# Kernel optimization log

Hardware: AMD Instinct MI355X
Metric: run time of the kernel (lower is better)

The kernel has to match this reference:

```python
import jax, jax.numpy as jnp
import numpy as np

N = 100000      # nodes
E = 1000000     # edges (before self loops)
F_IN = 128      # num_features
G = 512         # graphs in batch
NC = 10         # num_classes
EPS_BN = 1e-5
NEG_SLOPE = 0.2


def setup_inputs() -> dict:
    key = jax.random.key(0)
    ks = iter(jax.random.split(key, 40))
    rn = lambda shape, s=0.1: jax.random.normal(next(ks), shape, jnp.float32) * s
    inp = {
        "x": jax.random.normal(next(ks), (N, F_IN), jnp.float32),
        "edge_index": jax.random.randint(next(ks), (2, E), 0, N),
        "batch": jnp.sort(jax.random.randint(next(ks), (N,), 0, G)),
        "W1": rn((F_IN, 128)), "as1": rn((8, 16)), "ad1": rn((8, 16)), "b1": jnp.zeros((128,), jnp.float32),
        "g1": jnp.ones((128,), jnp.float32), "be1": jnp.zeros((128,), jnp.float32),
        "Wl1": rn((128, 16)), "bl1": jnp.zeros((16,), jnp.float32),
        "gl1": jnp.ones((16,), jnp.float32), "bel1": jnp.zeros((16,), jnp.float32),
        "W2": rn((16, 96)), "as2": rn((4, 24)), "ad2": rn((4, 24)), "b2": jnp.zeros((96,), jnp.float32),
        "g2": jnp.ones((96,), jnp.float32), "be2": jnp.zeros((96,), jnp.float32),
        "Wl2": rn((96, 24)), "bl2": jnp.zeros((24,), jnp.float32),
        "gl2": jnp.ones((24,), jnp.float32), "bel2": jnp.zeros((24,), jnp.float32),
        "W3": rn((24, 64)), "as3": rn((2, 32)), "ad3": rn((2, 32)), "b3": jnp.zeros((64,), jnp.float32),
        "g3": jnp.ones((64,), jnp.float32), "be3": jnp.zeros((64,), jnp.float32),
        # final classifier
        "Wo": rn((64, NC)), "bo": jnp.zeros((NC,), jnp.float32),
    }
    return inp


def _bn(h, gamma, beta):
    # training-mode BatchNorm1d: batch statistics, biased variance
    m = jnp.mean(h, axis=0)
    v = jnp.var(h, axis=0)
    return gamma * (h - m) * jax.lax.rsqrt(v + EPS_BN) + beta


def _gat(h_in, src, dst, W, a_src, a_dst, bias, n):
    heads, ch = a_src.shape
    h = (h_in @ W).reshape(n, heads, ch)                     # [N,H,C]
    alpha_s = jnp.sum(h * a_src, axis=-1)                    # [N,H]
    alpha_d = jnp.sum(h * a_dst, axis=-1)                    # [N,H]
    e = jax.nn.leaky_relu(alpha_s[src] + alpha_d[dst], NEG_SLOPE)   # [E,H]
    emax = jax.ops.segment_max(e, dst, num_segments=n)       # segment softmax over target
    e = jnp.exp(e - emax[dst])
    denom = jax.ops.segment_sum(e, dst, num_segments=n)
    alpha = e / (denom[dst] + 1e-16)                         # [E,H]
    msg = h[src] * alpha[:, :, None]                         # [E,H,C]
    out = jax.ops.segment_sum(msg, dst, num_segments=n)      # [N,H,C]
    return out.reshape(n, heads * ch) + bias


def reference(x, edge_index, batch,
              W1, as1, ad1, b1, g1, be1, Wl1, bl1, gl1, bel1,
              W2, as2, ad2, b2, g2, be2, Wl2, bl2, gl2, bel2,
              W3, as3, ad3, b3, g3, be3, Wo, bo):
    n = x.shape[0]
    loop = jnp.arange(n)
    src = jnp.concatenate([edge_index[0], loop])   # add self loops (PyG default)
    dst = jnp.concatenate([edge_index[1], loop])

    h = jax.nn.relu(_bn(_gat(x, src, dst, W1, as1, ad1, b1, n), g1, be1))
    h = jax.nn.relu(_bn(h @ Wl1 + bl1, gl1, bel1))
    h = jax.nn.relu(_bn(_gat(h, src, dst, W2, as2, ad2, b2, n), g2, be2))
    h = jax.nn.relu(_bn(h @ Wl2 + bl2, gl2, bel2))
    h = jax.nn.relu(_bn(_gat(h, src, dst, W3, as3, ad3, b3, n), g3, be3))

    # global mean pool over graphs
    counts = jax.ops.segment_sum(jnp.ones((n,), h.dtype), batch, num_segments=G)
    pooled = jax.ops.segment_sum(h, batch, num_segments=G) / jnp.maximum(counts, 1.0)[:, None]
    # dropout is identity in eval
    return pooled @ Wo + bo
```

## Files before the change

kernel.cpp:

```cpp
#include <hip/hip_runtime.h>

typedef unsigned short u16;
typedef unsigned int   u32;
typedef unsigned long long u64;
typedef __attribute__((ext_vector_type(8))) short short8;
typedef __attribute__((ext_vector_type(4))) float f32x4;

#define DEVI __device__ __forceinline__

#define NPB 256
#define SHB 8
#define BHB 64

DEVI float bf2f(u16 u){ union{u32 i; float f;} x; x.i = ((u32)u)<<16; return x.f; }
DEVI u16 f2bf(float f){ union{float f; u32 i;} x; x.f = f;
  u32 r = (x.i + 0x7FFFu + ((x.i>>16)&1u))>>16; return (u16)r; }
DEVI float lrelu(float x){ return x > 0.f ? x : 0.2f*x; }
DEVI float gload(const void* p, size_t i, int f32){
  return f32 ? ((const float*)p)[i] : bf2f(((const u16*)p)[i]);
}

__global__ __launch_bounds__(256) void k_init(const void* x, int* flag, float* stats, int nst){
  int i = blockIdx.x*256 + threadIdx.x;
  if (i < nst) stats[i] = 0.f;
  if (i == 0){
    const u16* p = (const u16*)x;
    int hits = 0;
    for (int j = 0; j < 512; j++){
      u16 e = (p[j] >> 7) & 0xFF;
      if (e >= 0xC0) hits++;
    }
    *flag = hits ? 1 : 0;
  }
}

__global__ __launch_bounds__(1024) void k_bhist(const int* ei, int E, int* hist, int NB){
  __shared__ int lh[512];
  for (int b = threadIdx.x; b < NB; b += 1024) lh[b] = 0;
  __syncthreads();
  for (int e = blockIdx.x*1024 + threadIdx.x; e < E; e += BHB*1024)
    atomicAdd(&lh[((u32)ei[E + e]) >> SHB], 1);
  __syncthreads();
  for (int b = threadIdx.x; b < NB; b += 1024) hist[blockIdx.x*NB + b] = lh[b];
}

__global__ __launch_bounds__(256) void k_btot(const int* hist, int* tot, int NB){
  int b = blockIdx.x*256 + threadIdx.x;
  if (b < NB){
    int s = 0;
    for (int j = 0; j < BHB; j++) s += hist[j*NB + b];
    tot[b] = s;
  }
}

__global__ __launch_bounds__(1024) void k_bbase(const int* tot, int* base, int* coff, int NB, int N){
  __shared__ int l[1024];
  int t = threadIdx.x;
  int v = (t < NB) ? tot[t] : 0;
  l[t] = v; __syncthreads();
  for (int s = 1; s < 1024; s <<= 1){
    int add = (t >= s) ? l[t - s] : 0;
    __syncthreads();
    l[t] += add;
    __syncthreads();
  }
  if (t < NB) base[t] = l[t] - v;
  if (t == 1023){ base[NB] = l[1023]; coff[N] = l[1023]; }
}

__global__ __launch_bounds__(256) void k_bcur(int* hist, const int* base, int NB){
  int b = blockIdx.x*256 + threadIdx.x;
  if (b < NB){
    int run = base[b];
    for (int j = 0; j < BHB; j++){
      int v = hist[j*NB + b];
      hist[j*NB + b] = run;
      run += v;
    }
  }
}

__global__ __launch_bounds__(1024) void k_bfill(const int* ei, int E, const int* hist,
                                                u64* tmp, int NB){
  __shared__ int cur[512];
  for (int b = threadIdx.x; b < NB; b += 1024) cur[b] = hist[blockIdx.x*NB + b];
  __syncthreads();
  for (int e = blockIdx.x*1024 + threadIdx.x; e < E; e += BHB*1024){
    int s = ei[e], d = ei[E + e];
    int p = atomicAdd(&cur[((u32)d) >> SHB], 1);
    tmp[p] = ((u64)(u32)d << 32) | (u32)s;
  }
}

__global__ __launch_bounds__(256) void k_cfill(const u64* tmp, const int* base,
                                               int* coff, int* csr, int N){
  __shared__ int cnt[NPB], start[NPB];
  int b = blockIdx.x, t = threadIdx.x;
  int p0 = base[b], p1 = base[b + 1];
  cnt[t] = 0;
  __syncthreads();
  for (int i = p0 + t; i < p1; i += 256)
    atomicAdd(&cnt[(int)(tmp[i] >> 32) & (NPB - 1)], 1);
  __syncthreads();
  if (t == 0){
    int run = p0;
    for (int j = 0; j < NPB; j++){ start[j] = run; run += cnt[j]; }
  }
  __syncthreads();
  {
    int node = b*NPB + t;
    if (node < N) coff[node] = start[t];
    cnt[t] = 0;
  }
  __syncthreads();
  for (int i = p0 + t; i < p1; i += 256){
    u64 pr = tmp[i];
    int dj = (int)(pr >> 32) & (NPB - 1);
    int r = atomicAdd(&cnt[dj], 1);
    csr[start[dj] + r] = (int)(u32)pr;
  }
}

__global__ __launch_bounds__(256) void k_prepW(const void* Wg, u16* Wt, const int* dflag){
  const int f32 = dflag[0];
  for (int i = blockIdx.x*256 + threadIdx.x; i < 128*128; i += gridDim.x*256){
    int k = i >> 7, nn = i & 127;
    Wt[nn*128 + k] = f2bf(gload(Wg, i, f32));
  }
}

__global__ __launch_bounds__(256) void k_mfma1(const void* x, const u16* __restrict__ Wt,
                                               u16* __restrict__ out, int n, const int* dflag){
  const int f32 = dflag[0];
  const int wave = threadIdx.x >> 6;
  const int lane = threadIdx.x & 63;
  const int l15 = lane & 15, q = lane >> 4;
  const int arow = blockIdx.x*64 + wave*16 + l15;
  const bool rok = arow < n;

  f32x4 acc[8];
  #pragma unroll
  for (int t = 0; t < 8; t++) acc[t] = {0.f, 0.f, 0.f, 0.f};

  #pragma unroll
  for (int kk = 0; kk < 4; kk++){
    short8 a = {0,0,0,0,0,0,0,0};
    if (rok){
      const int ko = kk*32 + q*8;
      if (f32){
        const float* xp = (const float*)x + (size_t)arow*128 + ko;
        float4 v0 = *(const float4*)xp;
        float4 v1 = *(const float4*)(xp + 4);
        a[0]=(short)f2bf(v0.x); a[1]=(short)f2bf(v0.y); a[2]=(short)f2bf(v0.z); a[3]=(short)f2bf(v0.w);
        a[4]=(short)f2bf(v1.x); a[5]=(short)f2bf(v1.y); a[6]=(short)f2bf(v1.z); a[7]=(short)f2bf(v1.w);
      } else {
        a = *(const short8*)((const u16*)x + (size_t)arow*128 + ko);
      }
    }
    #pragma unroll
    for (int t = 0; t < 8; t++){
      short8 b = *(const short8*)(Wt + (size_t)(l15 + 16*t)*128 + kk*32 + q*8);
      acc[t] = __builtin_amdgcn_mfma_f32_16x16x32_bf16(a, b, acc[t], 0, 0, 0);
    }
  }

  const int orow0 = blockIdx.x*64 + wave*16 + q*4;
  #pragma unroll
  for (int r = 0; r < 4; r++){
    int orow = orow0 + r;
    if (orow < n){
      #pragma unroll
      for (int t = 0; t < 8; t++)
        out[(size_t)orow*128 + l15 + 16*t] = f2bf(acc[t][r]);
    }
  }
}

__global__ __launch_bounds__(256) void k_alpha1(const u16* __restrict__ A, const void* a_s, const void* a_d,
    u16* als, u16* ald, int n, const int* dflag){
  const int f32 = dflag[0];
  int idx = blockIdx.x*256 + threadIdx.x;
  if (idx >= n*8) return;
  int r = idx >> 3, hd = idx & 7;
  const u16* p = A + (size_t)r*128 + hd*16;
  float s = 0.f, d = 0.f;
  #pragma unroll
  for (int c = 0; c < 16; c++){
    float v = bf2f(p[c]);
    s = fmaf(v, gload(a_s, hd*16 + c, f32), s);
    d = fmaf(v, gload(a_d, hd*16 + c, f32), d);
  }
  als[idx] = f2bf(s); ald[idx] = f2bf(d);
}

template<int K,int M,int H,int RT,int TPB,bool AFFINE,bool ALPHA>
__global__ __launch_bounds__(TPB) void k_gemm(
    const u16* in, const void* Wg,
    const float* stat, const void* gam, const void* bet, float invn,
    const void* a_s, const void* a_d, u16* out, u16* als, u16* ald, int n,
    const int* dflag)
{
  constexpr int CT = 4;
  constexpr int TC = M/CT;
  constexpr int TR = TPB/TC;
  constexpr int ROWS = TR*RT;
  constexpr int C = M/H;
  static_assert(TPB % TC == 0, "");
  __shared__ __align__(16) u16 Wl[K*M];
  __shared__ float Il[ROWS*(K+1)];
  __shared__ float red[ALPHA ? (2*ROWS*TC) : 1];
  __shared__ float faL[AFFINE ? K : 1], fdL[AFFINE ? K : 1];

  const int f32 = dflag[0];
  if constexpr (AFFINE){
    for (int k = threadIdx.x; k < K; k += TPB){
      float m = stat[k]*invn;
      float vv = stat[128 + k]*invn - m*m;
      float a = gload(gam, k, f32) * rsqrtf(vv + 1e-5f);
      faL[k] = a;
      fdL[k] = gload(bet, k, f32) - m*a;
    }
    __syncthreads();
  }

  for (int i = threadIdx.x; i < K*M; i += TPB)
    Wl[i] = f32 ? f2bf(((const float*)Wg)[i]) : ((const u16*)Wg)[i];

  const int rowbase = blockIdx.x * ROWS;
  for (int i = threadIdx.x; i < ROWS*K; i += TPB){
    int rr = i / K, k = i - rr*K;
    int r = rowbase + rr;
    float v = 0.f;
    if (r < n){
      v = bf2f(in[(size_t)r*K + k]);
      if constexpr (AFFINE) v = fmaxf(fmaf(faL[k], v, fdL[k]), 0.f);
    }
    Il[rr*(K+1) + k] = v;
  }
  __syncthreads();

  const int tc = threadIdx.x % TC;
  const int tr = threadIdx.x / TC;
  float acc[RT][CT];
  #pragma unroll
  for (int j = 0; j < RT; j++)
    #pragma unroll
    for (int c = 0; c < CT; c++) acc[j][c] = 0.f;

  #pragma unroll 8
  for (int k = 0; k < K; k++){
    ushort4 u = *(const ushort4*)&Wl[k*M + tc*CT];
    float w0 = bf2f(u.x), w1 = bf2f(u.y), w2 = bf2f(u.z), w3 = bf2f(u.w);
    #pragma unroll
    for (int j = 0; j < RT; j++){
      float iv = Il[(tr + j*TR)*(K+1) + k];
      acc[j][0] = fmaf(iv, w0, acc[j][0]);
      acc[j][1] = fmaf(iv, w1, acc[j][1]);
      acc[j][2] = fmaf(iv, w2, acc[j][2]);
      acc[j][3] = fmaf(iv, w3, acc[j][3]);
    }
  }

  #pragma unroll
  for (int j = 0; j < RT; j++){
    int r = rowbase + tr + j*TR;
    if (r < n){
      ushort4 st;
      st.x = f2bf(acc[j][0]); st.y = f2bf(acc[j][1]);
      st.z = f2bf(acc[j][2]); st.w = f2bf(acc[j][3]);
      *(ushort4*)&out[(size_t)r*M + tc*CT] = st;
    }
  }

  if constexpr (ALPHA){
    #pragma unroll
    for (int j = 0; j < RT; j++){
      float ps = 0.f, pd = 0.f;
      #pragma unroll
      for (int c = 0; c < CT; c++){
        ps = fmaf(acc[j][c], gload(a_s, tc*CT + c, f32), ps);
        pd = fmaf(acc[j][c], gload(a_d, tc*CT + c, f32), pd);
      }
      red[(tr + j*TR)*TC + tc] = ps;
      red[ROWS*TC + (tr + j*TR)*TC + tc] = pd;
    }
    __syncthreads();
    if (threadIdx.x < ROWS){
      int r = rowbase + threadIdx.x;
      if (r < n){
        float hs[H], hd[H];
        #pragma unroll
        for (int h = 0; h < H; h++){ hs[h] = 0.f; hd[h] = 0.f; }
        for (int t2 = 0; t2 < TC; t2++){
          int hh = (t2*CT)/C;
          hs[hh] += red[threadIdx.x*TC + t2];
          hd[hh] += red[ROWS*TC + threadIdx.x*TC + t2];
        }
        #pragma unroll
        for (int h = 0; h < H; h++){
          als[(size_t)r*H + h] = f2bf(hs[h]);
          ald[(size_t)r*H + h] = f2bf(hd[h]);
        }
      }
    }
  }
}

template<int H,int C>
__global__ __launch_bounds__(256) void k_pullA(const u16* __restrict__ h,
    const u16* __restrict__ als, const u16* __restrict__ ald,
    const int* __restrict__ off, const int* __restrict__ csr, u16* __restrict__ out, int n)
{
  constexpr int F = H*C;
  constexpr int L = F/2;
  int wid = blockIdx.x*4 + (threadIdx.x >> 6);
  if (wid >= n) return;
  int lane = threadIdx.x & 63;
  if (lane >= L) return;
  int hd = (2*lane)/C;
  float adi = bf2f(ald[(size_t)wid*H + hd]);
  float asi = bf2f(als[(size_t)wid*H + hd]);
  const u32* hw = (const u32*)h;

  float w = __expf(lrelu(asi + adi));
  u32 v = hw[(size_t)wid*L + lane];
  float a0 = w * bf2f((u16)v);
  float a1 = w * bf2f((u16)(v >> 16));
  float den = w;

  int e = off[wid], e1 = off[wid + 1];
  for (; e + 8 <= e1; e += 8){
    int s[8]; float bl[8]; u32 vv[8];
    #pragma unroll
    for (int u = 0; u < 8; u++) s[u] = csr[e + u];
    #pragma unroll
    for (int u = 0; u < 8; u++) bl[u] = bf2f(als[(size_t)s[u]*H + hd]);
    #pragma unroll
    for (int u = 0; u < 8; u++) vv[u] = hw[(size_t)s[u]*L + lane];
    #pragma unroll
    for (int u = 0; u < 8; u++){
      float wu = __expf(lrelu(bl[u] + adi));
      a0 = fmaf(wu, bf2f((u16)vv[u]), a0);
      a1 = fmaf(wu, bf2f((u16)(vv[u] >> 16)), a1);
      den += wu;
    }
  }
  if (e < e1){
    int s[8]; float bl[8]; u32 vv[8];
    #pragma unroll
    for (int u = 0; u < 8; u++){ int idx = e + u; s[u] = csr[idx < e1 ? idx : e]; }
    #pragma unroll
    for (int u = 0; u < 8; u++) bl[u] = bf2f(als[(size_t)s[u]*H + hd]);
    #pragma unroll
    for (int u = 0; u < 8; u++) vv[u] = hw[(size_t)s[u]*L + lane];
    #pragma unroll
    for (int u = 0; u < 8; u++){
      float wu = (e + u < e1) ? __expf(lrelu(bl[u] + adi)) : 0.f;
      a0 = fmaf(wu, bf2f((u16)vv[u]), a0);
      a1 = fmaf(wu, bf2f((u16)(vv[u] >> 16)), a1);
      den += wu;
    }
  }
  float r = 1.f/(den + 1e-16f);
  ((u32*)out)[(size_t)wid*L + lane] = (u32)f2bf(a0*r) | ((u32)f2bf(a1*r) << 16);
}

__global__ __launch_bounds__(256) void k_pullB(const u16* __restrict__ h,
    const u16* __restrict__ als, const u16* __restrict__ ald,
    const int* __restrict__ off, const int* __restrict__ csr, u16* __restrict__ out, int n)
{
  int wid = blockIdx.x*4 + (threadIdx.x >> 6);
  if (wid >= n) return;
  int lane = threadIdx.x & 63;
  int half = lane >> 5, fi = lane & 31;
  int hd = fi >> 4;
  float adi = bf2f(ald[(size_t)wid*2 + hd]);
  float asi = bf2f(als[(size_t)wid*2 + hd]);
  const u32* hw = (const u32*)h;

  float a0 = 0.f, a1 = 0.f, den = 0.f;
  if (half == 0){
    float w = __expf(lrelu(asi + adi));
    u32 v = hw[(size_t)wid*32 + fi];
    a0 = w * bf2f((u16)v);
    a1 = w * bf2f((u16)(v >> 16));
    den = w;
  }
  int e = off[wid] + half, e1 = off[wid + 1];
  for (; e + 6 < e1; e += 8){
    int s[4]; float bl[4]; u32 vv[4];
    #pragma unroll
    for (int u = 0; u < 4; u++) s[u] = csr[e + 2*u];
    #pragma unroll
    for (int u = 0; u < 4; u++) bl[u] = bf2f(als[(size_t)s[u]*2 + hd]);
    #pragma unroll
    for (int u = 0; u < 4; u++) vv[u] = hw[(size_t)s[u]*32 + fi];
    #pragma unroll
    for (int u = 0; u < 4; u++){
      float wu = __expf(lrelu(bl[u] + adi));
      a0 = fmaf(wu, bf2f((u16)vv[u]), a0);
      a1 = fmaf(wu, bf2f((u16)(vv[u] >> 16)), a1);
      den += wu;
    }
  }
  if (e < e1){
    int s[4]; float bl[4]; u32 vv[4];
    #pragma unroll
    for (int u = 0; u < 4; u++){ int idx = e + 2*u; s[u] = csr[idx < e1 ? idx : e]; }
    #pragma unroll
    for (int u = 0; u < 4; u++) bl[u] = bf2f(als[(size_t)s[u]*2 + hd]);
    #pragma unroll
    for (int u = 0; u < 4; u++) vv[u] = hw[(size_t)s[u]*32 + fi];
    #pragma unroll
    for (int u = 0; u < 4; u++){
      float wu = (e + 2*u < e1) ? __expf(lrelu(bl[u] + adi)) : 0.f;
      a0 = fmaf(wu, bf2f((u16)vv[u]), a0);
      a1 = fmaf(wu, bf2f((u16)(vv[u] >> 16)), a1);
      den += wu;
    }
  }
  a0 += __shfl_xor(a0, 32);
  a1 += __shfl_xor(a1, 32);
  den += __shfl_xor(den, 32);
  if (half == 0){
    float r = 1.f/(den + 1e-16f);
    ((u32*)out)[(size_t)wid*32 + fi] = (u32)f2bf(a0*r) | ((u32)f2bf(a1*r) << 16);
  }
}

template<int F,int TPB>
__global__ __launch_bounds__(TPB) void k_colstats(const u16* x, int n, float* s1, float* s2)
{
  constexpr int RPB = TPB/F;
  static_assert(TPB % F == 0, "");
  int tc = threadIdx.x % F;
  int tr = threadIdx.x / F;
  float a = 0.f, b = 0.f;
  for (int r = blockIdx.x*RPB + tr; r < n; r += gridDim.x*RPB){
    float v = bf2f(x[(size_t)r*F + tc]);
    a += v; b = fmaf(v, v, b);
  }
  __shared__ float l1[TPB], l2[TPB];
  l1[threadIdx.x] = a; l2[threadIdx.x] = b;
  __syncthreads();
  if (tr == 0){
    #pragma unroll
    for (int j = 1; j < RPB; j++){ a += l1[j*F + tc]; b += l2[j*F + tc]; }
    atomicAdd(&s1[tc], a); atomicAdd(&s2[tc], b);
  }
}

__global__ __launch_bounds__(256) void k_pool(const u16* B, const int* batch, int n,
    const float* stat, const void* g3, const void* be3, float invn,
    const void* Wo, const void* bo, void* outp, const int* dflag)
{
  const int f32 = dflag[0];
  __shared__ float fa[64], fd[64];
  if (threadIdx.x < 64){
    int k = threadIdx.x;
    float m = stat[k]*invn;
    float v = stat[128 + k]*invn - m*m;
    float a = gload(g3, k, f32) * rsqrtf(v + 1e-5f);
    fa[k] = a;
    fd[k] = gload(be3, k, f32) - m*a;
  }
  __syncthreads();

  int g = blockIdx.x;
  int lane = threadIdx.x & 63, wv = threadIdx.x >> 6;
  int s, e;
  { int l = 0, h = n; while (l < h){ int m = (l+h)>>1; if (batch[m] <  g) l = m+1; else h = m; } s = l; }
  { int l = s, h = n; while (l < h){ int m = (l+h)>>1; if (batch[m] <= g) l = m+1; else h = m; } e = l; }
  float a = fa[lane], d = fd[lane], acc = 0.f;
  for (int r = s + wv; r < e; r += 4)
    acc += fmaxf(fmaf(a, bf2f(B[(size_t)r*64 + lane]), d), 0.f);
  __shared__ float pl[4][64];
  pl[wv][lane] = acc;
  __syncthreads();
  if (wv == 0){
    float cnt = (e > s) ? (float)(e - s) : 1.f;
    pl[0][lane] = (pl[0][lane] + pl[1][lane] + pl[2][lane] + pl[3][lane]) / cnt;
  }
  __syncthreads();
  if (threadIdx.x < 10){
    int lo = threadIdx.x;
    float o = gload(bo, lo, f32);
    for (int l2 = 0; l2 < 64; l2++) o = fmaf(pl[0][l2], gload(Wo, l2*10 + lo, f32), o);
    if (f32) ((float*)outp)[g*10 + lo] = o;
    else     ((u16*) outp)[g*10 + lo] = f2bf(o);
  }
}

extern "C" void kernel_launch(void* const* d_in, const int* in_sizes, int n_in,
                              void* d_out, int out_size, void* d_ws, size_t ws_size,
                              hipStream_t stream)
{
  const void* x   = d_in[0];
  const int* ei   = (const int*)d_in[1];
  const int* batch= (const int*)d_in[2];
  const void* W1  = d_in[3];
  const void* as1 = d_in[4];
  const void* ad1 = d_in[5];
  const void* g1  = d_in[7];
  const void* be1 = d_in[8];
  const void* Wl1 = d_in[9];
  const void* gl1 = d_in[11];
  const void* bel1= d_in[12];
  const void* W2  = d_in[13];
  const void* as2 = d_in[14];
  const void* ad2 = d_in[15];
  const void* g2  = d_in[17];
  const void* be2 = d_in[18];
  const void* Wl2 = d_in[19];
  const void* gl2 = d_in[21];
  const void* bel2= d_in[22];
  const void* W3  = d_in[23];
  const void* as3 = d_in[24];
  const void* ad3 = d_in[25];
  const void* g3  = d_in[27];
  const void* be3 = d_in[28];
  const void* Wo  = d_in[29];
  const void* bo  = d_in[30];
  (void)n_in; (void)ws_size;

  const int N = in_sizes[2];
  const int E = in_sizes[1] / 2;
  const int G = out_size / 10;
  const int NB = (N + NPB - 1) >> SHB;

  char* w = (char*)d_ws;
  size_t off = 0;
  auto alloc = [&](size_t bytes)->void*{
    size_t o = off; off += (bytes + 255) & ~(size_t)255; return (void*)(w + o);
  };
  int*   dflag= (int*)alloc(4);
  int*   coff = (int*)alloc((size_t)(N+1)*4);
  int*   csr  = (int*)alloc((size_t)E*4);
  int*   bbase= (int*)alloc((size_t)(NB+1)*4);
  int*   tot  = (int*)alloc((size_t)NB*4);
  int*   hist = (int*)alloc((size_t)BHB*NB*4);
  float* stS  = (float*)alloc(1280*4);
  u16*   Wt   = (u16*)alloc(128*128*2);
  u16*   als  = (u16*)alloc((size_t)N*8*2);
  u16*   ald  = (u16*)alloc((size_t)N*8*2);
  u16*   Cb   = (u16*)alloc((size_t)N*24*2);
  u16*   A    = (u16*)alloc((size_t)N*128*2);
  u16*   B    = (u16*)alloc((size_t)N*128*2);
  u64*   tmp  = (u64*)A;

  const float invN = 1.f/(float)N;

  k_init<<<5, 256, 0, stream>>>(x, dflag, stS, 1280);
  k_prepW<<<16, 256, 0, stream>>>(W1, Wt, dflag);

  k_bhist<<<BHB, 1024, 0, stream>>>(ei, E, hist, NB);
  k_btot <<<(NB+255)/256, 256, 0, stream>>>(hist, tot, NB);
  k_bbase<<<1, 1024, 0, stream>>>(tot, bbase, coff, NB, N);
  k_bcur <<<(NB+255)/256, 256, 0, stream>>>(hist, bbase, NB);
  k_bfill<<<BHB, 1024, 0, stream>>>(ei, E, hist, tmp, NB);
  k_cfill<<<NB, 256, 0, stream>>>(tmp, bbase, coff, csr, N);

  k_mfma1<<<(N+63)/64, 256, 0, stream>>>(x, Wt, A, N, dflag);
  k_alpha1<<<(N*8+255)/256, 256, 0, stream>>>(A, as1, ad1, als, ald, N, dflag);
  k_pullA<8,16><<<(N+3)/4, 256, 0, stream>>>(A, als, ald, coff, csr, B, N);
  k_colstats<128,256><<<256, 256, 0, stream>>>(B, N, stS + 0, stS + 128);

  k_gemm<128,16,1,1,256,true,false><<<(N+63)/64, 256, 0, stream>>>(
      B, Wl1, stS + 0, g1, be1, invN, nullptr, nullptr, Cb, nullptr, nullptr, N, dflag);
  k_colstats<16,256><<<256, 256, 0, stream>>>(Cb, N, stS + 256, stS + 384);

  k_gemm<16,96,4,2,192,true,true><<<(N+15)/16, 192, 0, stream>>>(
      Cb, W2, stS + 256, gl1, bel1, invN, as2, ad2, A, als, ald, N, dflag);
  k_pullA<4,24><<<(N+3)/4, 256, 0, stream>>>(A, als, ald, coff, csr, B, N);
  k_colstats<96,192><<<256, 192, 0, stream>>>(B, N, stS + 512, stS + 640);

  k_gemm<96,24,1,2,192,true,false><<<(N+63)/64, 192, 0, stream>>>(
      B, Wl2, stS + 512, g2, be2, invN, nullptr, nullptr, Cb, nullptr, nullptr, N, dflag);
  k_colstats<24,192><<<256, 192, 0, stream>>>(Cb, N, stS + 768, stS + 896);

  k_gemm<24,64,2,2,256,true,true><<<(N+31)/32, 256, 0, stream>>>(
      Cb, W3, stS + 768, gl2, bel2, invN, as3, ad3, A, als, ald, N, dflag);
  k_pullB<<<(N+3)/4, 256, 0, stream>>>(A, als, ald, coff, csr, B, N);
  k_colstats<64,256><<<256, 256, 0, stream>>>(B, N, stS + 1024, stS + 1152);

  k_pool<<<G, 256, 0, stream>>>(B, batch, N, stS + 1024, g3, be3, invN, Wo, bo, d_out, dflag);
}
```

Baseline: 756.3 us.

## Share edge weights across wave lanes in GAT pull and merge CSR scan kernels

The GAT aggregation kernels are replaced by one templated kernel. Each lane computes the attention weight for one (edge, head) pair, and the source index and weight are broadcast to feature lanes by shuffles. This removes the redundant per-feature-lane exp and source-alpha loads, and it engages all 64 lanes even when the feature width is smaller than the wave. Attention logits are prescaled by log2(e) when stored, so the kernel can use the native exp2 instruction. Three small bucket prefix-scan kernels are merged into one launch. The cost is extra shuffle traffic and an inner loop with a variable trip count.

```diff
diff --git a/kernel.cpp b/kernel.cpp
--- a/kernel.cpp
+++ b/kernel.cpp
@@ -11,11 +11,13 @@
 #define NPB 256
 #define SHB 8
 #define BHB 64
+#define LOG2E 1.44269504088896340736f
 
 DEVI float bf2f(u16 u){ union{u32 i; float f;} x; x.i = ((u32)u)<<16; return x.f; }
 DEVI u16 f2bf(float f){ union{float f; u32 i;} x; x.f = f;
   u32 r = (x.i + 0x7FFFu + ((x.i>>16)&1u))>>16; return (u16)r; }
 DEVI float lrelu(float x){ return x > 0.f ? x : 0.2f*x; }
+DEVI float exp2g(float x){ return __builtin_amdgcn_exp2f(x); }
 DEVI float gload(const void* p, size_t i, int f32){
   return f32 ? ((const float*)p)[i] : bf2f(((const u16*)p)[i]);
 }
@@ -44,40 +46,25 @@
   for (int b = threadIdx.x; b < NB; b += 1024) hist[blockIdx.x*NB + b] = lh[b];
 }
 
-__global__ __launch_bounds__(256) void k_btot(const int* hist, int* tot, int NB){
-  int b = blockIdx.x*256 + threadIdx.x;
-  if (b < NB){
-    int s = 0;
-    for (int j = 0; j < BHB; j++) s += hist[j*NB + b];
-    tot[b] = s;
-  }
-}
-
-__global__ __launch_bounds__(1024) void k_bbase(const int* tot, int* base, int* coff, int NB, int N){
-  __shared__ int l[1024];
+__global__ __launch_bounds__(512) void k_bmid(int* hist, int* base, int* coff, int NB, int N){
+  __shared__ int l[512];
   int t = threadIdx.x;
-  int v = (t < NB) ? tot[t] : 0;
-  l[t] = v; __syncthreads();
-  for (int s = 1; s < 1024; s <<= 1){
-    int add = (t >= s) ? l[t - s] : 0;
+  int s = 0;
+  if (t < NB){ for (int j = 0; j < BHB; j++) s += hist[j*NB + t]; }
+  l[t] = s; __syncthreads();
+  for (int st = 1; st < 512; st <<= 1){
+    int a = (t >= st) ? l[t - st] : 0;
     __syncthreads();
-    l[t] += add;
+    l[t] += a;
     __syncthreads();
   }
-  if (t < NB) base[t] = l[t] - v;
-  if (t == 1023){ base[NB] = l[1023]; coff[N] = l[1023]; }
-}
-
-__global__ __launch_bounds__(256) void k_bcur(int* hist, const int* base, int NB){
-  int b = blockIdx.x*256 + threadIdx.x;
-  if (b < NB){
-    int run = base[b];
-    for (int j = 0; j < BHB; j++){
-      int v = hist[j*NB + b];
-      hist[j*NB + b] = run;
-      run += v;
-    }
-  }
+  int run0 = l[t] - s;
+  if (t < NB){
+    base[t] = run0;
+    int run = run0;
+    for (int j = 0; j < BHB; j++){ int v = hist[j*NB + t]; hist[j*NB + t] = run; run += v; }
+  }
+  if (t == 511){ base[NB] = l[511]; coff[N] = l[511]; }
 }
 
 __global__ __launch_bounds__(1024) void k_bfill(const int* ei, int E, const int* hist,
@@ -190,7 +177,7 @@
     s = fmaf(v, gload(a_s, hd*16 + c, f32), s);
     d = fmaf(v, gload(a_d, hd*16 + c, f32), d);
   }
-  als[idx] = f2bf(s); ald[idx] = f2bf(d);
+  als[idx] = f2bf(s * LOG2E); ald[idx] = f2bf(d * LOG2E);
 }
 
 template<int K,int M,int H,int RT,int TPB,bool AFFINE,bool ALPHA>
@@ -298,8 +285,8 @@
         }
         #pragma unroll
         for (int h = 0; h < H; h++){
-          als[(size_t)r*H + h] = f2bf(hs[h]);
-          ald[(size_t)r*H + h] = f2bf(hd[h]);
+          als[(size_t)r*H + h] = f2bf(hs[h] * LOG2E);
+          ald[(size_t)r*H + h] = f2bf(hd[h] * LOG2E);
         }
       }
     }
@@ -307,125 +294,63 @@
 }
 
 template<int H,int C>
-__global__ __launch_bounds__(256) void k_pullA(const u16* __restrict__ h,
+__global__ __launch_bounds__(256) void k_pullW(const u16* __restrict__ h,
     const u16* __restrict__ als, const u16* __restrict__ ald,
     const int* __restrict__ off, const int* __restrict__ csr, u16* __restrict__ out, int n)
 {
   constexpr int F = H*C;
   constexpr int L = F/2;
+  constexpr int LOGH = (H==8)?3:((H==4)?2:1);
+  constexpr int EPG = 64 >> LOGH;
   int wid = blockIdx.x*4 + (threadIdx.x >> 6);
   if (wid >= n) return;
   int lane = threadIdx.x & 63;
-  if (lane >= L) return;
-  int hd = (2*lane)/C;
-  float adi = bf2f(ald[(size_t)wid*H + hd]);
-  float asi = bf2f(als[(size_t)wid*H + hd]);
+  int uu = lane >> LOGH;
+  int hh = lane & (H-1);
+  int fl = (lane < L) ? lane : (L-1);
+  int hd = (2*fl)/C;
   const u32* hw = (const u32*)h;
 
-  float w = __expf(lrelu(asi + adi));
-  u32 v = hw[(size_t)wid*L + lane];
-  float a0 = w * bf2f((u16)v);
-  float a1 = w * bf2f((u16)(v >> 16));
-  float den = w;
-
-  int e = off[wid], e1 = off[wid + 1];
-  for (; e + 8 <= e1; e += 8){
-    int s[8]; float bl[8]; u32 vv[8];
-    #pragma unroll
-    for (int u = 0; u < 8; u++) s[u] = csr[e + u];
-    #pragma unroll
-    for (int u = 0; u < 8; u++) bl[u] = bf2f(als[(size_t)s[u]*H + hd]);
-    #pragma unroll
-    for (int u = 0; u < 8; u++) vv[u] = hw[(size_t)s[u]*L + lane];
-    #pragma unroll
-    for (int u = 0; u < 8; u++){
-      float wu = __expf(lrelu(bl[u] + adi));
-      a0 = fmaf(wu, bf2f((u16)vv[u]), a0);
-      a1 = fmaf(wu, bf2f((u16)(vv[u] >> 16)), a1);
-      den += wu;
-    }
-  }
-  if (e < e1){
-    int s[8]; float bl[8]; u32 vv[8];
-    #pragma unroll
-    for (int u = 0; u < 8; u++){ int idx = e + u; s[u] = csr[idx < e1 ? idx : e]; }
-    #pragma unroll
-    for (int u = 0; u < 8; u++) bl[u] = bf2f(als[(size_t)s[u]*H + hd]);
-    #pragma unroll
-    for (int u = 0; u < 8; u++) vv[u] = hw[(size_t)s[u]*L + lane];
-    #pragma unroll
-    for (int u = 0; u < 8; u++){
-      float wu = (e + u < e1) ? __expf(lrelu(bl[u] + adi)) : 0.f;
-      a0 = fmaf(wu, bf2f((u16)vv[u]), a0);
-      a1 = fmaf(wu, bf2f((u16)(vv[u] >> 16)), a1);
-      den += wu;
-    }
-  }
+  float adw = bf2f(ald[(u32)wid*H + hh]);
+  float wsw = exp2g(lrelu(bf2f(als[(u32)wid*H + hh]) + adw));
+  float den_lane = (uu == 0) ? wsw : 0.f;
+
+  float wsf = exp2g(lrelu(bf2f(als[(u32)wid*H + hd]) + bf2f(ald[(u32)wid*H + hd])));
+  u32 vs = hw[(u32)wid*L + fl];
+  float acc0 = wsf * bf2f((u16)vs);
+  float acc1 = wsf * bf2f((u16)(vs >> 16));
+
+  int e0 = off[wid], e1 = off[wid + 1];
+  for (int e = e0; e < e1; e += EPG){
+    int rem = e1 - e;
+    int su = csr[e + (uu < rem ? uu : 0)];
+    float w = exp2g(lrelu(bf2f(als[(u32)su*H + hh]) + adw));
+    if (uu >= rem) w = 0.f;
+    den_lane += w;
+    int cnt = rem < EPG ? rem : EPG;
+    for (int jj = 0; jj < cnt; jj += 8){
+      int sb[8]; float wb[8]; u32 vv[8];
+      #pragma unroll
+      for (int j = 0; j < 8; j++){
+        int sl = ((jj + j) << LOGH) + hd;
+        sb[j] = __shfl(su, sl);
+        wb[j] = __shfl(w,  sl);
+      }
+      #pragma unroll
+      for (int j = 0; j < 8; j++) vv[j] = hw[(u32)sb[j]*L + fl];
+      #pragma unroll
+      for (int j = 0; j < 8; j++){
+        acc0 = fmaf(wb[j], bf2f((u16)vv[j]), acc0);
+        acc1 = fmaf(wb[j], bf2f((u16)(vv[j] >> 16)), acc1);
+      }
+    }
+  }
+  #pragma unroll
+  for (int st = H; st < 64; st <<= 1) den_lane += __shfl_xor(den_lane, st);
+  float den = __shfl(den_lane, hd);
   float r = 1.f/(den + 1e-16f);
-  ((u32*)out)[(size_t)wid*L + lane] = (u32)f2bf(a0*r) | ((u32)f2bf(a1*r) << 16);
-}
-
-__global__ __launch_bounds__(256) void k_pullB(const u16* __restrict__ h,
-    const u16* __restrict__ als, const u16* __restrict__ ald,
-    const int* __restrict__ off, const int* __restrict__ csr, u16* __restrict__ out, int n)
-{
-  int wid = blockIdx.x*4 + (threadIdx.x >> 6);
-  if (wid >= n) return;
-  int lane = threadIdx.x & 63;
-  int half = lane >> 5, fi = lane & 31;
-  int hd = fi >> 4;
-  float adi = bf2f(ald[(size_t)wid*2 + hd]);
-  float asi = bf2f(als[(size_t)wid*2 + hd]);
-  const u32* hw = (const u32*)h;
-
-  float a0 = 0.f, a1 = 0.f, den = 0.f;
-  if (half == 0){
-    float w = __expf(lrelu(asi + adi));
-    u32 v = hw[(size_t)wid*32 + fi];
-    a0 = w * bf2f((u16)v);
-    a1 = w * bf2f((u16)(v >> 16));
-    den = w;
-  }
-  int e = off[wid] + half, e1 = off[wid + 1];
-  for (; e + 6 < e1; e += 8){
-    int s[4]; float bl[4]; u32 vv[4];
-    #pragma unroll
-    for (int u = 0; u < 4; u++) s[u] = csr[e + 2*u];
-    #pragma unroll
-    for (int u = 0; u < 4; u++) bl[u] = bf2f(als[(size_t)s[u]*2 + hd]);
-    #pragma unroll
-    for (int u = 0; u < 4; u++) vv[u] = hw[(size_t)s[u]*32 + fi];
-    #pragma unroll
-    for (int u = 0; u < 4; u++){
-      float wu = __expf(lrelu(bl[u] + adi));
-      a0 = fmaf(wu, bf2f((u16)vv[u]), a0);
-      a1 = fmaf(wu, bf2f((u16)(vv[u] >> 16)), a1);
-      den += wu;
-    }
-  }
-  if (e < e1){
-    int s[4]; float bl[4]; u32 vv[4];
-    #pragma unroll
-    for (int u = 0; u < 4; u++){ int idx = e + 2*u; s[u] = csr[idx < e1 ? idx : e]; }
-    #pragma unroll
-    for (int u = 0; u < 4; u++) bl[u] = bf2f(als[(size_t)s[u]*2 + hd]);
-    #pragma unroll
-    for (int u = 0; u < 4; u++) vv[u] = hw[(size_t)s[u]*32 + fi];
-    #pragma unroll
-    for (int u = 0; u < 4; u++){
-      float wu = (e + 2*u < e1) ? __expf(lrelu(bl[u] + adi)) : 0.f;
-      a0 = fmaf(wu, bf2f((u16)vv[u]), a0);
-      a1 = fmaf(wu, bf2f((u16)(vv[u] >> 16)), a1);
-      den += wu;
-    }
-  }
-  a0 += __shfl_xor(a0, 32);
-  a1 += __shfl_xor(a1, 32);
-  den += __shfl_xor(den, 32);
-  if (half == 0){
-    float r = 1.f/(den + 1e-16f);
-    ((u32*)out)[(size_t)wid*32 + fi] = (u32)f2bf(a0*r) | ((u32)f2bf(a1*r) << 16);
-  }
+  if (lane < L)
+    ((u32*)out)[(u32)wid*L + fl] = (u32)f2bf(acc0*r) | ((u32)f2bf(acc1*r) << 16);
 }
 
 template<int F,int TPB>
@@ -537,7 +462,6 @@
   int*   coff = (int*)alloc((size_t)(N+1)*4);
   int*   csr  = (int*)alloc((size_t)E*4);
   int*   bbase= (int*)alloc((size_t)(NB+1)*4);
-  int*   tot  = (int*)alloc((size_t)NB*4);
   int*   hist = (int*)alloc((size_t)BHB*NB*4);
   float* stS  = (float*)alloc(1280*4);
   u16*   Wt   = (u16*)alloc(128*128*2);
@@ -554,15 +478,13 @@
   k_prepW<<<16, 256, 0, stream>>>(W1, Wt, dflag);
 
   k_bhist<<<BHB, 1024, 0, stream>>>(ei, E, hist, NB);
-  k_btot <<<(NB+255)/256, 256, 0, stream>>>(hist, tot, NB);
-  k_bbase<<<1, 1024, 0, stream>>>(tot, bbase, coff, NB, N);
-  k_bcur <<<(NB+255)/256, 256, 0, stream>>>(hist, bbase, NB);
+  k_bmid <<<1, 512, 0, stream>>>(hist, bbase, coff, NB, N);
   k_bfill<<<BHB, 1024, 0, stream>>>(ei, E, hist, tmp, NB);
   k_cfill<<<NB, 256, 0, stream>>>(tmp, bbase, coff, csr, N);
 
   k_mfma1<<<(N+63)/64, 256, 0, stream>>>(x, Wt, A, N, dflag);
   k_alpha1<<<(N*8+255)/256, 256, 0, stream>>>(A, as1, ad1, als, ald, N, dflag);
-  k_pullA<8,16><<<(N+3)/4, 256, 0, stream>>>(A, als, ald, coff, csr, B, N);
+  k_pullW<8,16><<<(N+3)/4, 256, 0, stream>>>(A, als, ald, coff, csr, B, N);
   k_colstats<128,256><<<256, 256, 0, stream>>>(B, N, stS + 0, stS + 128);
 
   k_gemm<128,16,1,1,256,true,false><<<(N+63)/64, 256, 0, stream>>>(
@@ -571,7 +493,7 @@
 
   k_gemm<16,96,4,2,192,true,true><<<(N+15)/16, 192, 0, stream>>>(
       Cb, W2, stS + 256, gl1, bel1, invN, as2, ad2, A, als, ald, N, dflag);
-  k_pullA<4,24><<<(N+3)/4, 256, 0, stream>>>(A, als, ald, coff, csr, B, N);
+  k_pullW<4,24><<<(N+3)/4, 256, 0, stream>>>(A, als, ald, coff, csr, B, N);
   k_colstats<96,192><<<256, 192, 0, stream>>>(B, N, stS + 512, stS + 640);
 
   k_gemm<96,24,1,2,192,true,false><<<(N+63)/64, 192, 0, stream>>>(
@@ -580,7 +502,7 @@
 
   k_gemm<24,64,2,2,256,true,true><<<(N+31)/32, 256, 0, stream>>>(
       Cb, W3, stS + 768, gl2, bel2, invN, as3, ad3, A, als, ald, N, dflag);
-  k_pullB<<<(N+3)/4, 256, 0, stream>>>(A, als, ald, coff, csr, B, N);
+  k_pullW<2,32><<<(N+3)/4, 256, 0, stream>>>(A, als, ald, coff, csr, B, N);
   k_colstats<64,256><<<256, 256, 0, stream>>>(B, N, stS + 1024, stS + 1152);
 
   k_pool<<<G, 256, 0, stream>>>(B, batch, N, stS + 1024, g3, be3, invN, Wo, bo, d_out, dflag);
```

Measured after the change: 749.9 us. Within noise of the previous version (-0.8%).
